# Kernel optimization log

Measured on AMD Instinct MI355X. Metric: run time of the kernel, lower is better.

Reference implementation:

```python
import jax, jax.numpy as jnp
import numpy as np

MASK_IDX = 0

def setup_inputs() -> dict:
    key = jax.random.key(0)
    k1, k2 = jax.random.split(key)
    B, S, V = 16, 512, 32000
    # probabilities in (0,1); add tiny eps to avoid log(0)
    output = jax.random.uniform(k1, (B, S, V), dtype=jnp.float32, minval=1e-6, maxval=1.0)
    target = jax.random.randint(k2, (B, S), 0, V, dtype=jnp.int64)
    return {"output": output, "target": target}

def reference(output, target):
    # gather prob of the target class: [B, S]
    p = jnp.take_along_axis(output, target[..., None], axis=-1)[..., 0]
    mask = target != MASK_IDX
    nll = jnp.where(mask, -jnp.log(p), 0.0)
    count = jnp.sum(mask).astype(output.dtype)
    return jnp.sum(nll) / count
```

## Files before the change

kernel.cpp:

```cpp
#include <hip/hip_runtime.h>
#include <hip/hip_bf16.h>

#define MASK_IDX 0

__global__ __launch_bounds__(1024) void nll_loss_kernel(
    const float* __restrict__ out,
    const int*   __restrict__ tgt,
    float* __restrict__ res,
    int BS, int V)
{
    const int tid = threadIdx.x;

    float sum = 0.0f;
    float cnt = 0.0f;

    for (int i = tid; i < BS; i += blockDim.x) {
        int t = tgt[i];
        if (t != MASK_IDX) {
            float p = out[(long long)i * V + t];
            sum -= __builtin_logf(p);
            cnt += 1.0f;
        }
    }

    #pragma unroll
    for (int off = 32; off > 0; off >>= 1) {
        sum += __shfl_down(sum, off, 64);
        cnt += __shfl_down(cnt, off, 64);
    }

    __shared__ float ssum[16];
    __shared__ float scnt[16];
    const int wave = tid >> 6;
    const int lane = tid & 63;
    if (lane == 0) { ssum[wave] = sum; scnt[wave] = cnt; }
    __syncthreads();

    if (tid < 16) {
        sum = ssum[tid];
        cnt = scnt[tid];
        #pragma unroll
        for (int off = 8; off > 0; off >>= 1) {
            sum += __shfl_down(sum, off, 64);
            cnt += __shfl_down(cnt, off, 64);
        }
        if (tid == 0) {
            res[0] = sum / cnt;
        }
    }
}

extern "C" void kernel_launch(void* const* d_in, const int* in_sizes, int n_in,
                              void* d_out, int out_size, void* d_ws, size_t ws_size,
                              hipStream_t stream) {
    const float* out = (const float*)d_in[0];
    const int*   tgt = (const int*)d_in[1];
    float* res = (float*)d_out;

    const int BS = in_sizes[1];
    const int V  = in_sizes[0] / in_sizes[1];

    nll_loss_kernel<<<1, 1024, 0, stream>>>(out, tgt, res, BS, V);
}
```

Measured before the change: 1.102 ms.

## Split NLL gather across many single-wave blocks with two-pass reduction

Replaces the single 1024-thread block with BS/64 single-wave blocks, each gathering one target probability per thread and writing a (sum,count) partial to workspace. A second single-wave kernel reduces the partials and divides. This spreads the latency-bound scattered loads across all compute units instead of one, at the cost of an extra kernel launch and workspace traffic.

```diff
diff --git a/kernel.cpp b/kernel.cpp
--- a/kernel.cpp
+++ b/kernel.cpp
@@ -3,23 +3,22 @@
 
 #define MASK_IDX 0
 
-__global__ __launch_bounds__(1024) void nll_loss_kernel(
+__global__ __launch_bounds__(64) void nll_partial_kernel(
     const float* __restrict__ out,
     const int*   __restrict__ tgt,
-    float* __restrict__ res,
+    float2* __restrict__ partials,
     int BS, int V)
 {
-    const int tid = threadIdx.x;
+    const int i = blockIdx.x * 64 + threadIdx.x;
 
     float sum = 0.0f;
     float cnt = 0.0f;
-
-    for (int i = tid; i < BS; i += blockDim.x) {
-        int t = tgt[i];
+    if (i < BS) {
+        const int t = tgt[i];
         if (t != MASK_IDX) {
-            float p = out[(long long)i * V + t];
-            sum -= __builtin_logf(p);
-            cnt += 1.0f;
+            const float p = out[(long long)i * V + t];
+            sum = -__builtin_logf(p);
+            cnt = 1.0f;
         }
     }
 
@@ -29,24 +28,30 @@
         cnt += __shfl_down(cnt, off, 64);
     }
 
-    __shared__ float ssum[16];
-    __shared__ float scnt[16];
-    const int wave = tid >> 6;
-    const int lane = tid & 63;
-    if (lane == 0) { ssum[wave] = sum; scnt[wave] = cnt; }
-    __syncthreads();
+    if (threadIdx.x == 0) {
+        partials[blockIdx.x] = make_float2(sum, cnt);
+    }
+}
 
-    if (tid < 16) {
-        sum = ssum[tid];
-        cnt = scnt[tid];
-        #pragma unroll
-        for (int off = 8; off > 0; off >>= 1) {
-            sum += __shfl_down(sum, off, 64);
-            cnt += __shfl_down(cnt, off, 64);
-        }
-        if (tid == 0) {
-            res[0] = sum / cnt;
-        }
+__global__ __launch_bounds__(64) void nll_final_kernel(
+    const float2* __restrict__ partials,
+    float* __restrict__ res,
+    int nPart)
+{
+    float sum = 0.0f;
+    float cnt = 0.0f;
+    for (int j = threadIdx.x; j < nPart; j += 64) {
+        const float2 p = partials[j];
+        sum += p.x;
+        cnt += p.y;
+    }
+    #pragma unroll
+    for (int off = 32; off > 0; off >>= 1) {
+        sum += __shfl_down(sum, off, 64);
+        cnt += __shfl_down(cnt, off, 64);
+    }
+    if (threadIdx.x == 0) {
+        res[0] = sum / cnt;
     }
 }
 
@@ -56,9 +61,13 @@
     const float* out = (const float*)d_in[0];
     const int*   tgt = (const int*)d_in[1];
     float* res = (float*)d_out;
+    float2* partials = (float2*)d_ws;
 
     const int BS = in_sizes[1];
     const int V  = in_sizes[0] / in_sizes[1];
 
-    nll_loss_kernel<<<1, 1024, 0, stream>>>(out, tgt, res, BS, V);
+    const int nBlocks = (BS + 63) / 64;
+
+    nll_partial_kernel<<<nBlocks, 64, 0, stream>>>(out, tgt, partials, BS, V);
+    nll_final_kernel<<<1, 64, 0, stream>>>(partials, res, nBlocks);
 }
```

New measurement: 1.086 ms. Within noise of the previous version (-1.4%).
